# Kernel optimization log

Measured on AMD Instinct MI355X. Metric: run time of the kernel, lower is better.

Reference implementation:

```python
import jax, jax.numpy as jnp
import numpy as np

BN_EPS = 1e-5
SAMPLE_KEY = jax.random.key(42)


def setup_inputs() -> dict:
    key = jax.random.key(0)
    ks = jax.random.split(key, 12)
    B, W, E = 524288, 8, 4
    D = W * E  # 32, input dim of fc1

    def lin(k, fan_in, fan_out):
        k1, k2 = jax.random.split(k)
        bound = 1.0 / np.sqrt(fan_in)
        w = jax.random.uniform(k1, (fan_in, fan_out), jnp.float32, -bound, bound)
        b = jax.random.uniform(k2, (fan_out,), jnp.float32, -bound, bound)
        return w, b

    W1, b1 = lin(ks[0], D, 50)
    W2, b2 = lin(ks[1], 50, 30)
    W3, b3 = lin(ks[2], 30, 20)
    W4, b4 = lin(ks[3], 20, 15)
    W5, b5 = lin(ks[4], 15, W)
    # BatchNorm affine params (eval mode, running_mean=0, running_var=1)
    g1, be1 = jnp.ones((50,), jnp.float32), jnp.zeros((50,), jnp.float32)
    g2, be2 = jnp.ones((30,), jnp.float32), jnp.zeros((30,), jnp.float32)
    g3, be3 = jnp.ones((20,), jnp.float32), jnp.zeros((20,), jnp.float32)
    events = jax.random.normal(ks[5], (B, W, E), jnp.float32)
    return {"events": events,
            "W1": W1, "b1": b1, "g1": g1, "be1": be1,
            "W2": W2, "b2": b2, "g2": g2, "be2": be2,
            "W3": W3, "b3": b3, "g3": g3, "be3": be3,
            "W4": W4, "b4": b4, "W5": W5, "b5": b5}


def _bn_eval(x, g, b):
    # eval-mode BatchNorm1d with running_mean=0, running_var=1
    return x * (g / jnp.sqrt(1.0 + BN_EPS)) + b


def _probs(events, W1, b1, g1, be1, W2, b2, g2, be2, W3, b3, g3, be3, W4, b4, W5, b5):
    B = events.shape[0]
    x = events.reshape(B, -1)  # (B, window*event_size)
    h = jax.nn.relu(_bn_eval(x @ W1 + b1, g1, be1))
    h = jax.nn.relu(_bn_eval(h @ W2 + b2, g2, be2))
    h = jax.nn.relu(_bn_eval(h @ W3 + b3, g3, be3))
    h = jax.nn.relu(h @ W4 + b4)
    return jax.nn.sigmoid(h @ W5 + b5)  # (B, window_size)


def reference(events, W1, b1, g1, be1, W2, b2, g2, be2, W3, b3, g3, be3, W4, b4, W5, b5):
    p = _probs(events, W1, b1, g1, be1, W2, b2, g2, be2, W3, b3, g3, be3, W4, b4, W5, b5)
    # np.random.choice([0,1], p=[p, 1-p]) => P(choice=1) = 1 - p
    choice = jax.random.bernoulli(SAMPLE_KEY, 1.0 - p).astype(p.dtype)  # (B, W)
    chosen_events_np = 1.0 - choice
    flipped = jnp.abs(choice - p)            # prob of sampled outcome per element
    log_prob = jnp.log(jnp.prod(flipped, axis=1))  # (B,)
    return chosen_events_np, log_prob
```

## Files before the change

### kernel.cpp

```cpp
#include <hip/hip_runtime.h>
#include <math.h>

#define THREADS 256
#define TPW 4
#define ROWS_PER_BLOCK 256
#define P_MARGIN 2e-4f
#define FIXCAP 64

typedef float f32x4 __attribute__((ext_vector_type(4)));
typedef short short8 __attribute__((ext_vector_type(8)));
union Frag { unsigned u[4]; short8 s; };

#define FR1 0
#define FR2 2048
#define FR3 4096
#define FR4 5120
#define FR5 6144
#define VB1 6656
#define VS1 6708
#define VE1 6760
#define VB2 6812
#define VS2 6844
#define VE2 6876
#define VB3 6908
#define VS3 6928
#define VE3 6948
#define VB4 6968
#define VB5 6984
#define PZ  6992
#define WPOOL 7024

__device__ __forceinline__ void tf2x32(unsigned x0, unsigned x1,
                                       unsigned &o0, unsigned &o1) {
  const unsigned k0 = 0u;
  const unsigned k1 = 42u;
  const unsigned k2 = 0x1BD11BDAu ^ k0 ^ k1;
  x0 += k0; x1 += k1;
#define TF_R(r) { x0 += x1; x1 = (x1 << (r)) | (x1 >> (32 - (r))); x1 ^= x0; }
  TF_R(13) TF_R(15) TF_R(26) TF_R(6)
  x0 += k1; x1 += k2 + 1u;
  TF_R(17) TF_R(29) TF_R(16) TF_R(24)
  x0 += k2; x1 += k0 + 2u;
  TF_R(13) TF_R(15) TF_R(26) TF_R(6)
  x0 += k0; x1 += k1 + 3u;
  TF_R(17) TF_R(29) TF_R(16) TF_R(24)
  x0 += k1; x1 += k2 + 4u;
  TF_R(13) TF_R(15) TF_R(26) TF_R(6)
  x0 += k2; x1 += k0 + 5u;
#undef TF_R
  o0 = x0; o1 = x1;
}

__device__ __forceinline__ unsigned rtnb(float v) {
  unsigned b = __float_as_uint(v);
  return (b + 0x7FFFu + ((b >> 16) & 1u)) & 0xFFFF0000u;
}

__device__ __forceinline__ unsigned cvtpk(float a, float b) {
  unsigned r;
  asm("v_cvt_pk_bf16_f32 %0, %1, %2" : "=v"(r) : "v"(a), "v"(b));
  return r;
}

__device__ __forceinline__ void pack8(const float f[8], short8 &H, short8 &L) {
  Frag h, l;
#pragma unroll
  for (int d = 0; d < 4; ++d) {
    unsigned hd = cvtpk(f[2 * d], f[2 * d + 1]);
    h.u[d] = hd;
    float r0 = f[2 * d]     - __uint_as_float(hd << 16);
    float r1 = f[2 * d + 1] - __uint_as_float(hd & 0xFFFF0000u);
    l.u[d] = cvtpk(r0, r1);
  }
  H = h.s; L = l.s;
}

__device__ __forceinline__ f32x4 mfma16(short8 a, short8 b, f32x4 c) {
  return __builtin_amdgcn_mfma_f32_16x16x32_bf16(a, b, c, 0, 0, 0);
}

__device__ __forceinline__ short8 ldfrag(const float *sW, int dwoff) {
  return *reinterpret_cast<const short8 *>(sW + dwoff);
}
__device__ __forceinline__ f32x4 ldv4(const float *sW, int dwoff) {
  return *reinterpret_cast<const f32x4 *>(sW + dwoff);
}

template <int K, int N, int NT, int FB>
__device__ __forceinline__ void stageA(const float *__restrict__ W,
                                       unsigned short *hp, int t, bool perm) {
  for (int i = t; i < K * N; i += THREADS) {
    int k = i / N, n = i - k * N;
    float v = W[i];
    unsigned hb = rtnb(v);
    unsigned lb = rtnb(v - __uint_as_float(hb));
    int kt = k >> 5, g = (k >> 3) & 3, e = k & 7, d = e >> 1, par = e & 1;
    int tile, r;
    if (perm) {
      int pg = n >> 5, m = n & 31, tt = (m >> 2) & 1;
      r = ((m >> 3) << 2) | (m & 3);
      tile = pg * 2 + tt;
    } else {
      tile = n >> 4; r = n & 15;
    }
    int lane = g * 16 + r;
    int dwhi = FB + (kt * NT + tile) * 512 + lane * 4 + d;
    hp[2 * dwhi + par] = (unsigned short)(hb >> 16);
    hp[2 * (dwhi + 256) + par] = (unsigned short)(lb >> 16);
  }
}

__device__ __forceinline__ void build_image(
    float *img, int t,
    const float *W1, const float *b1, const float *g1, const float *be1,
    const float *W2, const float *b2, const float *g2, const float *be2,
    const float *W3, const float *b3, const float *g3, const float *be3,
    const float *W4, const float *b4, const float *W5, const float *b5) {
  const float rden = (float)(1.0 / sqrt(1.0 + 1e-5));
  for (int i = t; i < WPOOL; i += THREADS) img[i] = 0.f;
  __syncthreads();
  unsigned short *hp = reinterpret_cast<unsigned short *>(img);
  stageA<32, 50, 4, FR1>(W1, hp, t, true);
  stageA<50, 30, 2, FR2>(W2, hp, t, true);
  stageA<30, 20, 2, FR3>(W3, hp, t, true);
  stageA<20, 15, 2, FR4>(W4, hp, t, true);
  stageA<15,  8, 1, FR5>(W5, hp, t, false);
  if (t < 50)                  { img[VB1 + t] = b1[t]; img[VS1 + t] = g1[t] * rden; img[VE1 + t] = be1[t]; }
  else if (t >= 64 && t < 94)  { int i = t - 64;  img[VB2 + i] = b2[i]; img[VS2 + i] = g2[i] * rden; img[VE2 + i] = be2[i]; }
  else if (t >= 128 && t < 148){ int i = t - 128; img[VB3 + i] = b3[i]; img[VS3 + i] = g3[i] * rden; img[VE3 + i] = be3[i]; }
  else if (t >= 192 && t < 207){ img[VB4 + (t - 192)] = b4[t - 192]; }
  else if (t >= 224 && t < 232){ img[VB5 + (t - 224)] = b5[t - 224]; }
}

__global__ __launch_bounds__(THREADS, 1)
void pack_kernel(const float* __restrict__ W1, const float* __restrict__ b1,
                 const float* __restrict__ g1, const float* __restrict__ be1,
                 const float* __restrict__ W2, const float* __restrict__ b2,
                 const float* __restrict__ g2, const float* __restrict__ be2,
                 const float* __restrict__ W3, const float* __restrict__ b3,
                 const float* __restrict__ g3, const float* __restrict__ be3,
                 const float* __restrict__ W4, const float* __restrict__ b4,
                 const float* __restrict__ W5, const float* __restrict__ b5,
                 float* __restrict__ img) {
  build_image(img, threadIdx.x, W1, b1, g1, be1, W2, b2, g2, be2,
              W3, b3, g3, be3, W4, b4, W5, b5);
}

__global__ __launch_bounds__(THREADS, 2)
void wtf_kernel(const float* __restrict__ events,
                const float* __restrict__ W1, const float* __restrict__ b1,
                const float* __restrict__ g1, const float* __restrict__ be1,
                const float* __restrict__ W2, const float* __restrict__ b2,
                const float* __restrict__ g2, const float* __restrict__ be2,
                const float* __restrict__ W3, const float* __restrict__ b3,
                const float* __restrict__ g3, const float* __restrict__ be3,
                const float* __restrict__ W4, const float* __restrict__ b4,
                const float* __restrict__ W5, const float* __restrict__ b5,
                const float* __restrict__ img,
                float* __restrict__ out_chosen,
                float* __restrict__ out_logp,
                int B) {
  __shared__ float sW[WPOOL];
  __shared__ unsigned s_cnt;
  __shared__ unsigned s_rows[FIXCAP];
  __shared__ double sA[64];
  __shared__ double sB[64];
  __shared__ double sF[8];

  const int t = threadIdx.x;

  if (t == 0) s_cnt = 0;
  if (img) {
    const float4 *s4 = reinterpret_cast<const float4 *>(img);
    float4 *d4 = reinterpret_cast<float4 *>(sW);
    for (int i = t; i < WPOOL / 4; i += THREADS) d4[i] = s4[i];
  } else {
    build_image(sW, t, W1, b1, g1, be1, W2, b2, g2, be2,
                W3, b3, g3, be3, W4, b4, W5, b5);
  }
  __syncthreads();

  const int w = t >> 6, lane = t & 63;
  const int c = lane & 15, g = lane >> 4;
  const int labase = lane * 4;

  const short8 F4h0 = ldfrag(sW, FR4 + 0 * 512 + labase);
  const short8 F4l0 = ldfrag(sW, FR4 + 0 * 512 + 256 + labase);
  const short8 F4h1 = ldfrag(sW, FR4 + 1 * 512 + labase);
  const short8 F4l1 = ldfrag(sW, FR4 + 1 * 512 + 256 + labase);
  const short8 F5h  = ldfrag(sW, FR5 + labase);
  const short8 F5l  = ldfrag(sW, FR5 + 256 + labase);

  const int wrow0 = blockIdx.x * ROWS_PER_BLOCK + w * (TPW * 16);
  const float4 *xp = reinterpret_cast<const float4 *>(
      events + (size_t)(wrow0 + c) * 32 + g * 8);

  f32x4 aa[TPW];

#pragma unroll
  for (int tt = 0; tt < TPW; ++tt) {
    float4 xa = xp[tt * 128], xb = xp[tt * 128 + 1];
    float xf[8] = {xa.x, xa.y, xa.z, xa.w, xb.x, xb.y, xb.z, xb.w};
    short8 Xh, Xl; pack8(xf, Xh, Xl);

    f32x4 a1[4];
#pragma unroll
    for (int ti = 0; ti < 4; ++ti) {
      f32x4 acc = ldv4(sW, VB1 + (ti >> 1) * 32 + g * 8 + (ti & 1) * 4);
      short8 wh = ldfrag(sW, FR1 + ti * 512 + labase);
      short8 wl = ldfrag(sW, FR1 + ti * 512 + 256 + labase);
      acc = mfma16(wh, Xl, acc);
      acc = mfma16(wl, Xh, acc);
      a1[ti] = mfma16(wh, Xh, acc);
    }

    short8 B2h[2], B2l[2];
    {
      f32x4 sc0 = ldv4(sW, VS1 + g * 8),      of0 = ldv4(sW, VE1 + g * 8);
      f32x4 sc1 = ldv4(sW, VS1 + g * 8 + 4),  of1 = ldv4(sW, VE1 + g * 8 + 4);
      float f[8];
#pragma unroll
      for (int q = 0; q < 4; ++q) {
        f[q]     = fmaxf(fmaf(a1[0][q], sc0[q], of0[q]), 0.f);
        f[4 + q] = fmaxf(fmaf(a1[1][q], sc1[q], of1[q]), 0.f);
      }
      pack8(f, B2h[0], B2l[0]);
      f32x4 sc2 = ldv4(sW, VS1 + 32 + g * 8),     of2 = ldv4(sW, VE1 + 32 + g * 8);
      f32x4 sc3 = ldv4(sW, VS1 + 32 + g * 8 + 4), of3 = ldv4(sW, VE1 + 32 + g * 8 + 4);
#pragma unroll
      for (int q = 0; q < 4; ++q) {
        f[q]     = fmaxf(fmaf(a1[2][q], sc2[q], of2[q]), 0.f);
        f[4 + q] = fmaxf(fmaf(a1[3][q], sc3[q], of3[q]), 0.f);
      }
      pack8(f, B2h[1], B2l[1]);
    }

    f32x4 a2[2];
#pragma unroll
    for (int ti = 0; ti < 2; ++ti) {
      f32x4 acc = ldv4(sW, VB2 + g * 8 + ti * 4);
#pragma unroll
      for (int kt = 0; kt < 2; ++kt) {
        short8 wh = ldfrag(sW, FR2 + (kt * 2 + ti) * 512 + labase);
        short8 wl = ldfrag(sW, FR2 + (kt * 2 + ti) * 512 + 256 + labase);
        acc = mfma16(wh, B2l[kt], acc);
        acc = mfma16(wl, B2h[kt], acc);
        acc = mfma16(wh, B2h[kt], acc);
      }
      a2[ti] = acc;
    }

    short8 B3h, B3l;
    {
      f32x4 sc0 = ldv4(sW, VS2 + g * 8),     of0 = ldv4(sW, VE2 + g * 8);
      f32x4 sc1 = ldv4(sW, VS2 + g * 8 + 4), of1 = ldv4(sW, VE2 + g * 8 + 4);
      float f[8];
#pragma unroll
      for (int q = 0; q < 4; ++q) {
        f[q]     = fmaxf(fmaf(a2[0][q], sc0[q], of0[q]), 0.f);
        f[4 + q] = fmaxf(fmaf(a2[1][q], sc1[q], of1[q]), 0.f);
      }
      pack8(f, B3h, B3l);
    }

    f32x4 a3[2];
#pragma unroll
    for (int ti = 0; ti < 2; ++ti) {
      f32x4 acc = ldv4(sW, VB3 + g * 8 + ti * 4);
      short8 wh = ldfrag(sW, FR3 + ti * 512 + labase);
      short8 wl = ldfrag(sW, FR3 + ti * 512 + 256 + labase);
      acc = mfma16(wh, B3l, acc);
      acc = mfma16(wl, B3h, acc);
      a3[ti] = mfma16(wh, B3h, acc);
    }

    short8 B4h, B4l;
    {
      f32x4 sc0 = ldv4(sW, VS3 + g * 8),     of0 = ldv4(sW, VE3 + g * 8);
      f32x4 sc1 = ldv4(sW, VS3 + g * 8 + 4), of1 = ldv4(sW, VE3 + g * 8 + 4);
      float f[8];
#pragma unroll
      for (int q = 0; q < 4; ++q) {
        f[q]     = fmaxf(fmaf(a3[0][q], sc0[q], of0[q]), 0.f);
        f[4 + q] = fmaxf(fmaf(a3[1][q], sc1[q], of1[q]), 0.f);
      }
      pack8(f, B4h, B4l);
    }

    f32x4 a4[2];
    {
      f32x4 acc0 = ldv4(sW, VB4 + g * 8);
      acc0 = mfma16(F4h0, B4l, acc0);
      acc0 = mfma16(F4l0, B4h, acc0);
      a4[0] = mfma16(F4h0, B4h, acc0);
      f32x4 acc1 = ldv4(sW, VB4 + g * 8 + 4);
      acc1 = mfma16(F4h1, B4l, acc1);
      acc1 = mfma16(F4l1, B4h, acc1);
      a4[1] = mfma16(F4h1, B4h, acc1);
    }

    short8 B5h, B5l;
    {
      float f[8];
#pragma unroll
      for (int q = 0; q < 4; ++q) {
        f[q]     = fmaxf(a4[0][q], 0.f);
        f[4 + q] = fmaxf(a4[1][q], 0.f);
      }
      pack8(f, B5h, B5l);
    }

    {
      f32x4 acc = ldv4(sW, VB5 + g * 4);
      acc = mfma16(F5h, B5l, acc);
      acc = mfma16(F5l, B5h, acc);
      aa[tt] = mfma16(F5h, B5h, acc);
    }
  }

#pragma unroll
  for (int tt = 0; tt < TPW; ++tt) {
    const int row = wrow0 + tt * 16 + c;
    float s2v = __shfl_xor(aa[tt][2], 32);
    float s3v = __shfl_xor(aa[tt][3], 32);
    float l0 = (g < 2) ? aa[tt][0] : s2v;
    float l1 = (g < 2) ? aa[tt][1] : s3v;
    const int base = ((g & 1) << 2) | ((g >> 1) << 1);
    float p0 = 1.f / (1.f + __expf(-l0));
    float p1 = 1.f / (1.f + __expf(-l1));
    unsigned o0, o1, q0, q1;
    tf2x32(0u, 8u * (unsigned)row + (unsigned)base,      o0, o1);
    tf2x32(0u, 8u * (unsigned)row + (unsigned)base + 1u, q0, q1);
    float u0 = __uint_as_float(0x3F800000u | ((o0 ^ o1) >> 9)) - 1.f;
    float u1 = __uint_as_float(0x3F800000u | ((q0 ^ q1) >> 9)) - 1.f;
    float th0 = 1.f - p0, th1 = 1.f - p1;
    bool c0 = u0 < th0, c1 = u1 < th1;
    bool need = (fabsf(u0 - th0) < P_MARGIN) || (fabsf(u1 - th1) < P_MARGIN);
    float prod = (c0 ? th0 : p0) * (c1 ? th1 : p1);
    prod *= __shfl_xor(prod, 16);
    prod *= __shfl_xor(prod, 32);
    float2 chv = make_float2(c0 ? 0.f : 1.f, c1 ? 0.f : 1.f);
    *reinterpret_cast<float2 *>(out_chosen + (size_t)row * 8 + base) = chv;
    if (g == 0) out_logp[row] = __logf(prod);
    if (need) {
      unsigned i = atomicAdd(&s_cnt, 1u);
      if (i < FIXCAP) s_rows[i] = (unsigned)row;
    }
  }

  __syncthreads();
  unsigned cnt = s_cnt;
  if (cnt > FIXCAP) cnt = FIXCAP;
  if (cnt == 0) return;

  const double denom = sqrt(1.0 + 1e-5);
  for (unsigned r = 0; r < cnt; ++r) {
    const int rb = (int)s_rows[r];

    if (t < 32) sA[t] = (double)events[(size_t)rb * 32 + t];
    __syncthreads();

    double v = 0.0;
    if (t < 50) {
#pragma unroll
      for (int k = 0; k < 32; ++k) v = fma(sA[k], (double)W1[k * 50 + t], v);
      v += (double)b1[t];
      v = v * ((double)g1[t] / denom) + (double)be1[t];
      v = v > 0.0 ? v : 0.0;
    }
    __syncthreads();
    if (t < 50) sB[t] = v;
    __syncthreads();

    v = 0.0;
    if (t < 30) {
#pragma unroll
      for (int k = 0; k < 50; ++k) v = fma(sB[k], (double)W2[k * 30 + t], v);
      v += (double)b2[t];
      v = v * ((double)g2[t] / denom) + (double)be2[t];
      v = v > 0.0 ? v : 0.0;
    }
    __syncthreads();
    if (t < 30) sA[t] = v;
    __syncthreads();

    v = 0.0;
    if (t < 20) {
#pragma unroll
      for (int k = 0; k < 30; ++k) v = fma(sA[k], (double)W3[k * 20 + t], v);
      v += (double)b3[t];
      v = v * ((double)g3[t] / denom) + (double)be3[t];
      v = v > 0.0 ? v : 0.0;
    }
    __syncthreads();
    if (t < 20) sB[t] = v;
    __syncthreads();

    v = 0.0;
    if (t < 15) {
#pragma unroll
      for (int k = 0; k < 20; ++k) v = fma(sB[k], (double)W4[k * 15 + t], v);
      v += (double)b4[t];
      v = v > 0.0 ? v : 0.0;
    }
    __syncthreads();
    if (t < 15) sA[t] = v;
    __syncthreads();

    if (t < 8) {
      v = 0.0;
#pragma unroll
      for (int k = 0; k < 15; ++k) v = fma(sA[k], (double)W5[k * 8 + t], v);
      v += (double)b5[t];
      double p = 1.0 / (1.0 + exp(-v));
      unsigned j = 8u * (unsigned)rb + (unsigned)t, o0, o1;
      tf2x32(0u, j, o0, o1);
      unsigned bits = o0 ^ o1;
      float u = __uint_as_float(0x3F800000u | (bits >> 9)) - 1.f;
      double thr = 1.0 - p;
      bool choice = ((double)u < thr);
      out_chosen[(size_t)rb * 8 + t] = choice ? 0.f : 1.f;
      sF[t] = choice ? thr : p;
    }
    __syncthreads();
    if (t == 0) {
      double prod = 1.0;
      for (int w2 = 0; w2 < 8; ++w2) prod *= sF[w2];
      out_logp[rb] = (float)log(prod);
    }
    __syncthreads();
  }
}

extern "C" void kernel_launch(void* const* d_in, const int* in_sizes, int n_in,
                              void* d_out, int out_size, void* d_ws, size_t ws_size,
                              hipStream_t stream) {
  const float* events = (const float*)d_in[0];
  const float* W1  = (const float*)d_in[1];
  const float* b1  = (const float*)d_in[2];
  const float* g1  = (const float*)d_in[3];
  const float* be1 = (const float*)d_in[4];
  const float* W2  = (const float*)d_in[5];
  const float* b2  = (const float*)d_in[6];
  const float* g2  = (const float*)d_in[7];
  const float* be2 = (const float*)d_in[8];
  const float* W3  = (const float*)d_in[9];
  const float* b3  = (const float*)d_in[10];
  const float* g3  = (const float*)d_in[11];
  const float* be3 = (const float*)d_in[12];
  const float* W4  = (const float*)d_in[13];
  const float* b4  = (const float*)d_in[14];
  const float* W5  = (const float*)d_in[15];
  const float* b5  = (const float*)d_in[16];

  const int B = in_sizes[0] / 32;
  float* out = (float*)d_out;
  float* out_chosen = out;
  float* out_logp   = out + (size_t)B * 8;

  float* img = (ws_size >= (size_t)WPOOL * sizeof(float)) ? (float*)d_ws
                                                          : nullptr;
  if (img) {
    hipLaunchKernelGGL(pack_kernel, dim3(1), dim3(THREADS), 0, stream,
                       W1, b1, g1, be1, W2, b2, g2, be2,
                       W3, b3, g3, be3, W4, b4, W5, b5, img);
  }

  const int blocks = (B + ROWS_PER_BLOCK - 1) / ROWS_PER_BLOCK;
  hipLaunchKernelGGL(wtf_kernel, dim3(blocks), dim3(THREADS), 0, stream,
                     events, W1, b1, g1, be1, W2, b2, g2, be2,
                     W3, b3, g3, be3, W4, b4, W5, b5,
                     img, out_chosen, out_logp, B);
}
```

Measured before the change: 222.8 us.

## Interleave two row tiles per iteration to reuse weight fragments and hide MFMA latency

The per-tile MLP loop now processes two 16-row tiles together. Each weight fragment and bias loaded from LDS is shared by both tiles, and the two tiles' independent MFMA chains are interleaved so the dependent accumulation latency can overlap. Launch bounds drop from two blocks per CU to one, which allows more registers for the doubled live state but lowers occupancy.

```diff
diff --git a/kernel.cpp b/kernel.cpp
--- a/kernel.cpp
+++ b/kernel.cpp
@@ -146,7 +146,7 @@
               W3, b3, g3, be3, W4, b4, W5, b5);
 }
 
-__global__ __launch_bounds__(THREADS, 2)
+__global__ __launch_bounds__(THREADS, 1)
 void wtf_kernel(const float* __restrict__ events,
                 const float* __restrict__ W1, const float* __restrict__ b1,
                 const float* __restrict__ g1, const float* __restrict__ be1,
@@ -198,123 +198,158 @@
   f32x4 aa[TPW];
 
 #pragma unroll
-  for (int tt = 0; tt < TPW; ++tt) {
-    float4 xa = xp[tt * 128], xb = xp[tt * 128 + 1];
-    float xf[8] = {xa.x, xa.y, xa.z, xa.w, xb.x, xb.y, xb.z, xb.w};
-    short8 Xh, Xl; pack8(xf, Xh, Xl);
-
-    f32x4 a1[4];
+  for (int it = 0; it < TPW / 2; ++it) {
+    short8 Xh[2], Xl[2];
+    {
+      float4 xa0 = xp[(2 * it + 0) * 128], xb0 = xp[(2 * it + 0) * 128 + 1];
+      float4 xa1 = xp[(2 * it + 1) * 128], xb1 = xp[(2 * it + 1) * 128 + 1];
+      float f0[8] = {xa0.x, xa0.y, xa0.z, xa0.w, xb0.x, xb0.y, xb0.z, xb0.w};
+      float f1[8] = {xa1.x, xa1.y, xa1.z, xa1.w, xb1.x, xb1.y, xb1.z, xb1.w};
+      pack8(f0, Xh[0], Xl[0]);
+      pack8(f1, Xh[1], Xl[1]);
+    }
+
+    f32x4 a1[2][4];
 #pragma unroll
     for (int ti = 0; ti < 4; ++ti) {
-      f32x4 acc = ldv4(sW, VB1 + (ti >> 1) * 32 + g * 8 + (ti & 1) * 4);
       short8 wh = ldfrag(sW, FR1 + ti * 512 + labase);
       short8 wl = ldfrag(sW, FR1 + ti * 512 + 256 + labase);
-      acc = mfma16(wh, Xl, acc);
-      acc = mfma16(wl, Xh, acc);
-      a1[ti] = mfma16(wh, Xh, acc);
-    }
-
-    short8 B2h[2], B2l[2];
+      f32x4 bias = ldv4(sW, VB1 + (ti >> 1) * 32 + g * 8 + (ti & 1) * 4);
+#pragma unroll
+      for (int u = 0; u < 2; ++u) {
+        f32x4 acc = bias;
+        acc = mfma16(wh, Xl[u], acc);
+        acc = mfma16(wl, Xh[u], acc);
+        a1[u][ti] = mfma16(wh, Xh[u], acc);
+      }
+    }
+
+    short8 B2h[2][2], B2l[2][2];
     {
       f32x4 sc0 = ldv4(sW, VS1 + g * 8),      of0 = ldv4(sW, VE1 + g * 8);
       f32x4 sc1 = ldv4(sW, VS1 + g * 8 + 4),  of1 = ldv4(sW, VE1 + g * 8 + 4);
-      float f[8];
-#pragma unroll
-      for (int q = 0; q < 4; ++q) {
-        f[q]     = fmaxf(fmaf(a1[0][q], sc0[q], of0[q]), 0.f);
-        f[4 + q] = fmaxf(fmaf(a1[1][q], sc1[q], of1[q]), 0.f);
-      }
-      pack8(f, B2h[0], B2l[0]);
       f32x4 sc2 = ldv4(sW, VS1 + 32 + g * 8),     of2 = ldv4(sW, VE1 + 32 + g * 8);
       f32x4 sc3 = ldv4(sW, VS1 + 32 + g * 8 + 4), of3 = ldv4(sW, VE1 + 32 + g * 8 + 4);
 #pragma unroll
-      for (int q = 0; q < 4; ++q) {
-        f[q]     = fmaxf(fmaf(a1[2][q], sc2[q], of2[q]), 0.f);
-        f[4 + q] = fmaxf(fmaf(a1[3][q], sc3[q], of3[q]), 0.f);
-      }
-      pack8(f, B2h[1], B2l[1]);
-    }
-
-    f32x4 a2[2];
+      for (int u = 0; u < 2; ++u) {
+        float f[8];
+#pragma unroll
+        for (int q = 0; q < 4; ++q) {
+          f[q]     = fmaxf(fmaf(a1[u][0][q], sc0[q], of0[q]), 0.f);
+          f[4 + q] = fmaxf(fmaf(a1[u][1][q], sc1[q], of1[q]), 0.f);
+        }
+        pack8(f, B2h[u][0], B2l[u][0]);
+#pragma unroll
+        for (int q = 0; q < 4; ++q) {
+          f[q]     = fmaxf(fmaf(a1[u][2][q], sc2[q], of2[q]), 0.f);
+          f[4 + q] = fmaxf(fmaf(a1[u][3][q], sc3[q], of3[q]), 0.f);
+        }
+        pack8(f, B2h[u][1], B2l[u][1]);
+      }
+    }
+
+    f32x4 a2[2][2];
+#pragma unroll
+    for (int u = 0; u < 2; ++u) {
+      a2[u][0] = ldv4(sW, VB2 + g * 8);
+      a2[u][1] = ldv4(sW, VB2 + g * 8 + 4);
+    }
 #pragma unroll
     for (int ti = 0; ti < 2; ++ti) {
-      f32x4 acc = ldv4(sW, VB2 + g * 8 + ti * 4);
 #pragma unroll
       for (int kt = 0; kt < 2; ++kt) {
         short8 wh = ldfrag(sW, FR2 + (kt * 2 + ti) * 512 + labase);
         short8 wl = ldfrag(sW, FR2 + (kt * 2 + ti) * 512 + 256 + labase);
-        acc = mfma16(wh, B2l[kt], acc);
-        acc = mfma16(wl, B2h[kt], acc);
-        acc = mfma16(wh, B2h[kt], acc);
-      }
-      a2[ti] = acc;
-    }
-
-    short8 B3h, B3l;
+#pragma unroll
+        for (int u = 0; u < 2; ++u) {
+          a2[u][ti] = mfma16(wh, B2l[u][kt], a2[u][ti]);
+          a2[u][ti] = mfma16(wl, B2h[u][kt], a2[u][ti]);
+          a2[u][ti] = mfma16(wh, B2h[u][kt], a2[u][ti]);
+        }
+      }
+    }
+
+    short8 B3h[2], B3l[2];
     {
       f32x4 sc0 = ldv4(sW, VS2 + g * 8),     of0 = ldv4(sW, VE2 + g * 8);
       f32x4 sc1 = ldv4(sW, VS2 + g * 8 + 4), of1 = ldv4(sW, VE2 + g * 8 + 4);
-      float f[8];
-#pragma unroll
-      for (int q = 0; q < 4; ++q) {
-        f[q]     = fmaxf(fmaf(a2[0][q], sc0[q], of0[q]), 0.f);
-        f[4 + q] = fmaxf(fmaf(a2[1][q], sc1[q], of1[q]), 0.f);
-      }
-      pack8(f, B3h, B3l);
-    }
-
-    f32x4 a3[2];
+#pragma unroll
+      for (int u = 0; u < 2; ++u) {
+        float f[8];
+#pragma unroll
+        for (int q = 0; q < 4; ++q) {
+          f[q]     = fmaxf(fmaf(a2[u][0][q], sc0[q], of0[q]), 0.f);
+          f[4 + q] = fmaxf(fmaf(a2[u][1][q], sc1[q], of1[q]), 0.f);
+        }
+        pack8(f, B3h[u], B3l[u]);
+      }
+    }
+
+    f32x4 a3[2][2];
 #pragma unroll
     for (int ti = 0; ti < 2; ++ti) {
-      f32x4 acc = ldv4(sW, VB3 + g * 8 + ti * 4);
       short8 wh = ldfrag(sW, FR3 + ti * 512 + labase);
       short8 wl = ldfrag(sW, FR3 + ti * 512 + 256 + labase);
-      acc = mfma16(wh, B3l, acc);
-      acc = mfma16(wl, B3h, acc);
-      a3[ti] = mfma16(wh, B3h, acc);
-    }
-
-    short8 B4h, B4l;
+      f32x4 bias = ldv4(sW, VB3 + g * 8 + ti * 4);
+#pragma unroll
+      for (int u = 0; u < 2; ++u) {
+        f32x4 acc = bias;
+        acc = mfma16(wh, B3l[u], acc);
+        acc = mfma16(wl, B3h[u], acc);
+        a3[u][ti] = mfma16(wh, B3h[u], acc);
+      }
+    }
+
+    short8 B4h[2], B4l[2];
     {
       f32x4 sc0 = ldv4(sW, VS3 + g * 8),     of0 = ldv4(sW, VE3 + g * 8);
       f32x4 sc1 = ldv4(sW, VS3 + g * 8 + 4), of1 = ldv4(sW, VE3 + g * 8 + 4);
+#pragma unroll
+      for (int u = 0; u < 2; ++u) {
+        float f[8];
+#pragma unroll
+        for (int q = 0; q < 4; ++q) {
+          f[q]     = fmaxf(fmaf(a3[u][0][q], sc0[q], of0[q]), 0.f);
+          f[4 + q] = fmaxf(fmaf(a3[u][1][q], sc1[q], of1[q]), 0.f);
+        }
+        pack8(f, B4h[u], B4l[u]);
+      }
+    }
+
+    f32x4 a4[2][2];
+#pragma unroll
+    for (int u = 0; u < 2; ++u) {
+      f32x4 acc0 = ldv4(sW, VB4 + g * 8);
+      acc0 = mfma16(F4h0, B4l[u], acc0);
+      acc0 = mfma16(F4l0, B4h[u], acc0);
+      a4[u][0] = mfma16(F4h0, B4h[u], acc0);
+      f32x4 acc1 = ldv4(sW, VB4 + g * 8 + 4);
+      acc1 = mfma16(F4h1, B4l[u], acc1);
+      acc1 = mfma16(F4l1, B4h[u], acc1);
+      a4[u][1] = mfma16(F4h1, B4h[u], acc1);
+    }
+
+    short8 B5h[2], B5l[2];
+#pragma unroll
+    for (int u = 0; u < 2; ++u) {
       float f[8];
 #pragma unroll
       for (int q = 0; q < 4; ++q) {
-        f[q]     = fmaxf(fmaf(a3[0][q], sc0[q], of0[q]), 0.f);
-        f[4 + q] = fmaxf(fmaf(a3[1][q], sc1[q], of1[q]), 0.f);
-      }
-      pack8(f, B4h, B4l);
-    }
-
-    f32x4 a4[2];
+        f[q]     = fmaxf(a4[u][0][q], 0.f);
+        f[4 + q] = fmaxf(a4[u][1][q], 0.f);
+      }
+      pack8(f, B5h[u], B5l[u]);
+    }
+
     {
-      f32x4 acc0 = ldv4(sW, VB4 + g * 8);
-      acc0 = mfma16(F4h0, B4l, acc0);
-      acc0 = mfma16(F4l0, B4h, acc0);
-      a4[0] = mfma16(F4h0, B4h, acc0);
-      f32x4 acc1 = ldv4(sW, VB4 + g * 8 + 4);
-      acc1 = mfma16(F4h1, B4l, acc1);
-      acc1 = mfma16(F4l1, B4h, acc1);
-      a4[1] = mfma16(F4h1, B4h, acc1);
-    }
-
-    short8 B5h, B5l;
-    {
-      float f[8];
-#pragma unroll
-      for (int q = 0; q < 4; ++q) {
-        f[q]     = fmaxf(a4[0][q], 0.f);
-        f[4 + q] = fmaxf(a4[1][q], 0.f);
-      }
-      pack8(f, B5h, B5l);
-    }
-
-    {
-      f32x4 acc = ldv4(sW, VB5 + g * 4);
-      acc = mfma16(F5h, B5l, acc);
-      acc = mfma16(F5l, B5h, acc);
-      aa[tt] = mfma16(F5h, B5h, acc);
+      f32x4 bias = ldv4(sW, VB5 + g * 4);
+#pragma unroll
+      for (int u = 0; u < 2; ++u) {
+        f32x4 acc = bias;
+        acc = mfma16(F5h, B5l[u], acc);
+        acc = mfma16(F5l, B5h[u], acc);
+        aa[2 * it + u] = mfma16(F5h, B5h[u], acc);
+      }
     }
   }
 
```

After: 246.0 us. 10.4% more time.

## Drop pack kernel, build weights per block, preload fragments, raise occupancy

Applied to the files above, without the earlier changes.

Removes the separate single-block pack kernel and its launch, so every block builds the shared-memory weight image straight from the raw parameters. Inside the tile loop, the W1/W2/W3 fragment loads from shared memory are issued ahead of the MFMA chains so LDS latency can overlap with the input load and earlier layers. The launch-bounds minimum blocks per CU is raised from 2 to 3 to encourage higher occupancy. The trade-offs are repeated per-block global reads and conversion work for the weight image, and more register pressure from the hoisted fragments under a tighter register budget, which could cause spills.

```diff
diff --git a/kernel.cpp b/kernel.cpp
--- a/kernel.cpp
+++ b/kernel.cpp
@@ -132,21 +132,7 @@
   else if (t >= 224 && t < 232){ img[VB5 + (t - 224)] = b5[t - 224]; }
 }
 
-__global__ __launch_bounds__(THREADS, 1)
-void pack_kernel(const float* __restrict__ W1, const float* __restrict__ b1,
-                 const float* __restrict__ g1, const float* __restrict__ be1,
-                 const float* __restrict__ W2, const float* __restrict__ b2,
-                 const float* __restrict__ g2, const float* __restrict__ be2,
-                 const float* __restrict__ W3, const float* __restrict__ b3,
-                 const float* __restrict__ g3, const float* __restrict__ be3,
-                 const float* __restrict__ W4, const float* __restrict__ b4,
-                 const float* __restrict__ W5, const float* __restrict__ b5,
-                 float* __restrict__ img) {
-  build_image(img, threadIdx.x, W1, b1, g1, be1, W2, b2, g2, be2,
-              W3, b3, g3, be3, W4, b4, W5, b5);
-}
-
-__global__ __launch_bounds__(THREADS, 2)
+__global__ __launch_bounds__(THREADS, 3)
 void wtf_kernel(const float* __restrict__ events,
                 const float* __restrict__ W1, const float* __restrict__ b1,
                 const float* __restrict__ g1, const float* __restrict__ be1,
@@ -156,7 +142,6 @@
                 const float* __restrict__ g3, const float* __restrict__ be3,
                 const float* __restrict__ W4, const float* __restrict__ b4,
                 const float* __restrict__ W5, const float* __restrict__ b5,
-                const float* __restrict__ img,
                 float* __restrict__ out_chosen,
                 float* __restrict__ out_logp,
                 int B) {
@@ -170,14 +155,8 @@
   const int t = threadIdx.x;
 
   if (t == 0) s_cnt = 0;
-  if (img) {
-    const float4 *s4 = reinterpret_cast<const float4 *>(img);
-    float4 *d4 = reinterpret_cast<float4 *>(sW);
-    for (int i = t; i < WPOOL / 4; i += THREADS) d4[i] = s4[i];
-  } else {
-    build_image(sW, t, W1, b1, g1, be1, W2, b2, g2, be2,
-                W3, b3, g3, be3, W4, b4, W5, b5);
-  }
+  build_image(sW, t, W1, b1, g1, be1, W2, b2, g2, be2,
+              W3, b3, g3, be3, W4, b4, W5, b5);
   __syncthreads();
 
   const int w = t >> 6, lane = t & 63;
@@ -199,19 +178,38 @@
 
 #pragma unroll
   for (int tt = 0; tt < TPW; ++tt) {
+    short8 W1h[4], W1l[4];
+#pragma unroll
+    for (int ti = 0; ti < 4; ++ti) {
+      W1h[ti] = ldfrag(sW, FR1 + ti * 512 + labase);
+      W1l[ti] = ldfrag(sW, FR1 + ti * 512 + 256 + labase);
+    }
+
     float4 xa = xp[tt * 128], xb = xp[tt * 128 + 1];
     float xf[8] = {xa.x, xa.y, xa.z, xa.w, xb.x, xb.y, xb.z, xb.w};
     short8 Xh, Xl; pack8(xf, Xh, Xl);
 
+    short8 W2h[4], W2l[4];
+#pragma unroll
+    for (int q = 0; q < 4; ++q) {
+      W2h[q] = ldfrag(sW, FR2 + q * 512 + labase);
+      W2l[q] = ldfrag(sW, FR2 + q * 512 + 256 + labase);
+    }
+
     f32x4 a1[4];
 #pragma unroll
     for (int ti = 0; ti < 4; ++ti) {
       f32x4 acc = ldv4(sW, VB1 + (ti >> 1) * 32 + g * 8 + (ti & 1) * 4);
-      short8 wh = ldfrag(sW, FR1 + ti * 512 + labase);
-      short8 wl = ldfrag(sW, FR1 + ti * 512 + 256 + labase);
-      acc = mfma16(wh, Xl, acc);
-      acc = mfma16(wl, Xh, acc);
-      a1[ti] = mfma16(wh, Xh, acc);
+      acc = mfma16(W1h[ti], Xl, acc);
+      acc = mfma16(W1l[ti], Xh, acc);
+      a1[ti] = mfma16(W1h[ti], Xh, acc);
+    }
+
+    short8 W3h[2], W3l[2];
+#pragma unroll
+    for (int ti = 0; ti < 2; ++ti) {
+      W3h[ti] = ldfrag(sW, FR3 + ti * 512 + labase);
+      W3l[ti] = ldfrag(sW, FR3 + ti * 512 + 256 + labase);
     }
 
     short8 B2h[2], B2l[2];
@@ -241,11 +239,9 @@
       f32x4 acc = ldv4(sW, VB2 + g * 8 + ti * 4);
 #pragma unroll
       for (int kt = 0; kt < 2; ++kt) {
-        short8 wh = ldfrag(sW, FR2 + (kt * 2 + ti) * 512 + labase);
-        short8 wl = ldfrag(sW, FR2 + (kt * 2 + ti) * 512 + 256 + labase);
-        acc = mfma16(wh, B2l[kt], acc);
-        acc = mfma16(wl, B2h[kt], acc);
-        acc = mfma16(wh, B2h[kt], acc);
+        acc = mfma16(W2h[kt * 2 + ti], B2l[kt], acc);
+        acc = mfma16(W2l[kt * 2 + ti], B2h[kt], acc);
+        acc = mfma16(W2h[kt * 2 + ti], B2h[kt], acc);
       }
       a2[ti] = acc;
     }
@@ -267,11 +263,9 @@
 #pragma unroll
     for (int ti = 0; ti < 2; ++ti) {
       f32x4 acc = ldv4(sW, VB3 + g * 8 + ti * 4);
-      short8 wh = ldfrag(sW, FR3 + ti * 512 + labase);
-      short8 wl = ldfrag(sW, FR3 + ti * 512 + 256 + labase);
-      acc = mfma16(wh, B3l, acc);
-      acc = mfma16(wl, B3h, acc);
-      a3[ti] = mfma16(wh, B3h, acc);
+      acc = mfma16(W3h[ti], B3l, acc);
+      acc = mfma16(W3l[ti], B3h, acc);
+      a3[ti] = mfma16(W3h[ti], B3h, acc);
     }
 
     short8 B4h, B4l;
@@ -458,17 +452,9 @@
   float* out_chosen = out;
   float* out_logp   = out + (size_t)B * 8;
 
-  float* img = (ws_size >= (size_t)WPOOL * sizeof(float)) ? (float*)d_ws
-                                                          : nullptr;
-  if (img) {
-    hipLaunchKernelGGL(pack_kernel, dim3(1), dim3(THREADS), 0, stream,
-                       W1, b1, g1, be1, W2, b2, g2, be2,
-                       W3, b3, g3, be3, W4, b4, W5, b5, img);
-  }
-
   const int blocks = (B + ROWS_PER_BLOCK - 1) / ROWS_PER_BLOCK;
   hipLaunchKernelGGL(wtf_kernel, dim3(blocks), dim3(THREADS), 0, stream,
                      events, W1, b1, g1, be1, W2, b2, g2, be2,
                      W3, b3, g3, be3, W4, b4, W5, b5,
-                     img, out_chosen, out_logp, B);
-}
+                     out_chosen, out_logp, B);
+}
```

Result: no change. 221.3 us (-0.7%).
